# Kernel tuning notes

Measured on AMD Instinct MI355X. Metric: run time of the kernel, lower is better.

The kernel has to match this reference:

```python
import jax, jax.numpy as jnp
import numpy as np

D_HIDDEN = 1024
N_HEADS = 16
D_HEAD = 64
B, N = 4, 1024
EPS = 1e-5


def _lin(x, w, b):
    # torch Linear: y = x @ W^T + b, w: [out, in]
    return jnp.einsum('...i,oi->...o', x, w) + b


def _ln(x, g, b):
    m = jnp.mean(x, axis=-1, keepdims=True)
    v = jnp.mean(jnp.square(x - m), axis=-1, keepdims=True)
    return (x - m) * jax.lax.rsqrt(v + EPS) * g + b


def setup_inputs() -> dict:
    key = jax.random.key(0)
    ks = jax.random.split(key, 20)
    d = D_HIDDEN
    s = 0.02
    inp = {
        'x': jax.random.normal(ks[0], (B, N, d), jnp.float32),
        'time_emb': jax.random.normal(ks[1], (B, d), jnp.float32),
        'ln1_g': jnp.ones((d,), jnp.float32),
        'ln1_b': jnp.zeros((d,), jnp.float32),
        's1_w': jax.random.normal(ks[2], (d, d), jnp.float32) * s,
        's1_b': jnp.zeros((d,), jnp.float32),
        'o1_w': jax.random.normal(ks[3], (d, d), jnp.float32) * s,
        'o1_b': jnp.zeros((d,), jnp.float32),
        'qkv_w': jax.random.normal(ks[4], (3 * d, d), jnp.float32) * s,
        'qkv_b': jnp.zeros((3 * d,), jnp.float32),
        'proj_w': jax.random.normal(ks[5], (d, d), jnp.float32) * s,
        'proj_b': jnp.zeros((d,), jnp.float32),
        'ln2_g': jnp.ones((d,), jnp.float32),
        'ln2_b': jnp.zeros((d,), jnp.float32),
        's2_w': jax.random.normal(ks[6], (d, d), jnp.float32) * s,
        's2_b': jnp.zeros((d,), jnp.float32),
        'o2_w': jax.random.normal(ks[7], (d, d), jnp.float32) * s,
        'o2_b': jnp.zeros((d,), jnp.float32),
        'up_w': jax.random.normal(ks[8], (4 * d, d), jnp.float32) * s,
        'up_b': jnp.zeros((4 * d,), jnp.float32),
        'down_w': jax.random.normal(ks[9], (d, 4 * d), jnp.float32) * s,
        'down_b': jnp.zeros((d,), jnp.float32),
    }
    return inp


def reference(x, time_emb, ln1_g, ln1_b, s1_w, s1_b, o1_w, o1_b,
              qkv_w, qkv_b, proj_w, proj_b, ln2_g, ln2_b,
              s2_w, s2_b, o2_w, o2_b, up_w, up_b, down_w, down_b):
    d = D_HIDDEN

    def ada(h, sw, sb, ow, ob):
        scale = _lin(time_emb, sw, sb)[:, None, :]   # [B,1,d]
        offset = _lin(time_emb, ow, ob)[:, None, :]
        return (1.0 + scale) * h + offset

    # attention branch
    h = ada(_ln(x, ln1_g, ln1_b), s1_w, s1_b, o1_w, o1_b)
    qkv = _lin(h, qkv_w, qkv_b)                       # [B,N,3d]
    q, k, v = jnp.split(qkv, 3, axis=-1)
    q = q.reshape(B, N, N_HEADS, D_HEAD)
    k = k.reshape(B, N, N_HEADS, D_HEAD)
    v = v.reshape(B, N, N_HEADS, D_HEAD)
    wei = jnp.einsum('bnhd,bmhd->bhnm', q, k) * (D_HEAD ** -0.5)
    wei = jax.nn.softmax(wei, axis=-1)
    attn = jnp.einsum('bhnm,bmhd->bnhd', wei, v).reshape(B, N, d)
    x = x + _lin(attn, proj_w, proj_b)

    # mlp branch (torch nn.GELU default = exact erf gelu)
    h = ada(_ln(x, ln2_g, ln2_b), s2_w, s2_b, o2_w, o2_b)
    h = jax.nn.gelu(_lin(h, up_w, up_b), approximate=False)
    x = x + _lin(h, down_w, down_b)
    return x, time_emb
```

## Files before the change

kernel.cpp:

```cpp
#include <hip/hip_runtime.h>
#include <hip/hip_bf16.h>
#include <math.h>

#define DH 1024
#define BB 4
#define NN 1024
#define NH 16
#define HD 64

typedef __attribute__((ext_vector_type(8))) short bf16x8;
typedef __attribute__((ext_vector_type(4))) float f32x4;
typedef __attribute__((ext_vector_type(4))) unsigned int u32x4;
typedef unsigned short u16;
typedef unsigned int u32;

static __device__ __forceinline__ u16 f2bf(float f) {
  __hip_bfloat16 h = __float2bfloat16(f);
  return *reinterpret_cast<u16*>(&h);
}
static __device__ __forceinline__ float bf2f(u16 x) {
  return __uint_as_float((unsigned)x << 16);
}

#define MFMA16(a, b, c) __builtin_amdgcn_mfma_f32_16x16x32_bf16(a, b, c, 0, 0, 0)
#define VMCNT(n) asm volatile("s_waitcnt vmcnt(" #n ")" ::: "memory")
#define MEMFENCE asm volatile("" ::: "memory")
#define BAR() do { __builtin_amdgcn_s_barrier(); MEMFENCE; } while (0)

static __device__ __forceinline__ void async16(const void* g, void* l) {
  __builtin_amdgcn_global_load_lds(
      (const __attribute__((address_space(1))) void*)g,
      (__attribute__((address_space(3))) void*)l, 16, 0, 0);
}

__global__ void cvt_all_kernel(const float* __restrict__ wq, const float* __restrict__ wp,
                               const float* __restrict__ wu, const float* __restrict__ wd,
                               u16* __restrict__ oq, u16* __restrict__ op,
                               u16* __restrict__ ou, u16* __restrict__ od) {
  int i = blockIdx.x * 256 + threadIdx.x;
  const float* src; u16* dst; int off;
  if (i < 786432)            { src = wq; dst = oq; off = i; }
  else if (i < 1048576)      { src = wp; dst = op; off = i - 786432; }
  else if (i < 2097152)      { src = wu; dst = ou; off = i - 1048576; }
  else                       { src = wd; dst = od; off = i - 2097152; }
  float4 v = reinterpret_cast<const float4*>(src)[off];
  ushort4 o;
  o.x = f2bf(v.x); o.y = f2bf(v.y); o.z = f2bf(v.z); o.w = f2bf(v.w);
  reinterpret_cast<ushort4*>(dst)[off] = o;
}

__global__ __launch_bounds__(256) void adaln_kernel(
    const float* __restrict__ e,
    const float* __restrict__ w_s1, const float* __restrict__ b_s1,
    const float* __restrict__ w_o1, const float* __restrict__ b_o1,
    const float* __restrict__ w_s2, const float* __restrict__ b_s2,
    const float* __restrict__ w_o2, const float* __restrict__ b_o2,
    float* __restrict__ out) {
  int tid = threadIdx.x, wid = tid >> 6, lane = tid & 63;
  int mat = blockIdx.y;
  const float* w; const float* bs; float addc;
  if (mat == 0)      { w = w_s1; bs = b_s1; addc = 1.f; }
  else if (mat == 1) { w = w_o1; bs = b_o1; addc = 0.f; }
  else if (mat == 2) { w = w_s2; bs = b_s2; addc = 1.f; }
  else               { w = w_o2; bs = b_o2; addc = 0.f; }
  int col = blockIdx.x * 4 + wid;
  float a0 = 0.f, a1 = 0.f, a2 = 0.f, a3 = 0.f;
  const float* wc_ = w + (size_t)col * DH;
  for (int i = 0; i < 16; ++i) {
    int k = i * 64 + lane;
    float wv = wc_[k];
    a0 += wv * e[k];
    a1 += wv * e[DH + k];
    a2 += wv * e[2 * DH + k];
    a3 += wv * e[3 * DH + k];
  }
  #pragma unroll
  for (int msk = 32; msk; msk >>= 1) {
    a0 += __shfl_xor(a0, msk); a1 += __shfl_xor(a1, msk);
    a2 += __shfl_xor(a2, msk); a3 += __shfl_xor(a3, msk);
  }
  if (lane == 0) {
    float bb = bs[col] + addc;
    out[mat * (4 * DH) + 0 * DH + col] = a0 + bb;
    out[mat * (4 * DH) + 1 * DH + col] = a1 + bb;
    out[mat * (4 * DH) + 2 * DH + col] = a2 + bb;
    out[mat * (4 * DH) + 3 * DH + col] = a3 + bb;
  }
}

__global__ __launch_bounds__(256) void ln_mod_kernel(
    const float* __restrict__ x, const float* __restrict__ g, const float* __restrict__ bta,
    const float* __restrict__ sp, const float* __restrict__ off, u16* __restrict__ out) {
  int row = blockIdx.x;
  int b = row >> 10;
  int tid = threadIdx.x;
  int wid = tid >> 6, lane = tid & 63;
  const float4 xv = reinterpret_cast<const float4*>(x + (size_t)row * DH)[tid];
  float s = xv.x + xv.y + xv.z + xv.w;
  float ss = xv.x * xv.x + xv.y * xv.y + xv.z * xv.z + xv.w * xv.w;
  #pragma unroll
  for (int m = 32; m; m >>= 1) { s += __shfl_xor(s, m); ss += __shfl_xor(ss, m); }
  __shared__ float red[8];
  if (lane == 0) { red[wid] = s; red[4 + wid] = ss; }
  __syncthreads();
  s = red[0] + red[1] + red[2] + red[3];
  ss = red[4] + red[5] + red[6] + red[7];
  float mean = s * (1.f / DH);
  float var = ss * (1.f / DH) - mean * mean;
  float rstd = rsqrtf(var + 1e-5f);
  int c = tid * 4;
  const float* spb = sp + b * DH + c;
  const float* offb = off + b * DH + c;
  float y0 = (xv.x - mean) * rstd * g[c + 0] + bta[c + 0];
  float y1 = (xv.y - mean) * rstd * g[c + 1] + bta[c + 1];
  float y2 = (xv.z - mean) * rstd * g[c + 2] + bta[c + 2];
  float y3 = (xv.w - mean) * rstd * g[c + 3] + bta[c + 3];
  ushort4 o;
  o.x = f2bf(spb[0] * y0 + offb[0]);
  o.y = f2bf(spb[1] * y1 + offb[1]);
  o.z = f2bf(spb[2] * y2 + offb[2]);
  o.w = f2bf(spb[3] * y3 + offb[3]);
  reinterpret_cast<ushort4*>(out + (size_t)row * DH)[tid] = o;
}

enum { EPI_BF16 = 0, EPI_GELU = 1, EPI_PART = 2, EPI_RES = 3 };

template <int EPI>
__global__ __launch_bounds__(512, 2) void gemmT_kernel(
    const u16* __restrict__ A, const u16* __restrict__ W,
    const float* __restrict__ bias, const float* __restrict__ resid,
    void* __restrict__ outp, int N, int K) {
  extern __shared__ u16 lds[];
  u16* Ab = lds;
  u16* Bb = lds + 24576;
  int tid = threadIdx.x;
  int wid = tid >> 6, lane = tid & 63;
  int l15 = lane & 15, l4 = lane >> 4;
  int wr = wid >> 2, wc = wid & 3;

  int nwg = gridDim.x * gridDim.y;
  int lin = blockIdx.y * gridDim.x + blockIdx.x;
  int q8 = nwg >> 3;
  int lin2 = (lin & 7) * q8 + (lin >> 3);
  int bx = lin2 % gridDim.x, by = lin2 / gridDim.x;
  int m0 = by * 256, n0 = bx * 128;
  int k0 = blockIdx.z * 1024;

  f32x4 acc[8][2] = {};

  const u16* Abase = A + (size_t)m0 * K + k0;
  const u16* Wbase = W + (size_t)n0 * K + k0;
  int i0 = tid, i1 = 512 + tid;
  int r0 = i0 >> 2, c0 = (i0 & 3) ^ ((r0 >> 1) & 3);
  int r1 = i1 >> 2, c1 = (i1 & 3) ^ ((r1 >> 1) & 3);
  int rB = tid >> 2, cB = (tid & 3) ^ ((rB >> 1) & 3);
  size_t gA0 = (size_t)r0 * K + c0 * 8;
  size_t gA1 = (size_t)r1 * K + c1 * 8;
  size_t gB0 = (size_t)rB * K + cB * 8;
  int lbA0 = (wid * 64) * 8;
  int lbA1 = (512 + wid * 64) * 8;

  auto stage = [&](int tt, int bi) {
    int qa = bi * 8192, qb = bi * 4096;
    const u16* Ak = Abase + tt * 32;
    const u16* Wk = Wbase + tt * 32;
    async16(Ak + gA0, &Ab[qa + lbA0]);
    async16(Ak + gA1, &Ab[qa + lbA1]);
    async16(Wk + gB0, &Bb[qb + lbA0]);
  };

  auto compute = [&](int bi) {
    int qa = bi * 8192, qb = bi * 4096;
    bf16x8 af[8], bfr[2];
    #pragma unroll
    for (int m = 0; m < 8; ++m) {
      int row = wr * 128 + m * 16 + l15;
      int ps = l4 ^ ((row >> 1) & 3);
      af[m] = *reinterpret_cast<const bf16x8*>(&Ab[qa + row * 32 + ps * 8]);
    }
    #pragma unroll
    for (int n = 0; n < 2; ++n) {
      int row = wc * 32 + n * 16 + l15;
      int ps = l4 ^ ((row >> 1) & 3);
      bfr[n] = *reinterpret_cast<const bf16x8*>(&Bb[qb + row * 32 + ps * 8]);
    }
    #pragma unroll
    for (int m = 0; m < 8; ++m)
      #pragma unroll
      for (int n = 0; n < 2; ++n)
        acc[m][n] = MFMA16(af[m], bfr[n], acc[m][n]);
  };

  stage(0, 0);
  stage(1, 1);
  for (int tb = 0; tb < 30; tb += 3) {
    VMCNT(3); BAR(); stage(tb + 2, 2); compute(0);
    VMCNT(3); BAR(); stage(tb + 3, 0); compute(1);
    VMCNT(3); BAR(); stage(tb + 4, 1); compute(2);
  }
  VMCNT(3); BAR(); compute(0);
  VMCNT(0); BAR(); compute(1);

  int M = gridDim.y * 256;
  u16* pout = (u16*)outp + (size_t)blockIdx.z * M * N;
  #pragma unroll
  for (int n = 0; n < 2; ++n) {
    int col = n0 + wc * 32 + n * 16 + l15;
    float bv = (EPI == EPI_PART) ? 0.f : bias[col];
    #pragma unroll
    for (int m = 0; m < 8; ++m) {
      #pragma unroll
      for (int r = 0; r < 4; ++r) {
        int rowg = m0 + wr * 128 + m * 16 + l4 * 4 + r;
        float v = acc[m][n][r] + bv;
        if (EPI == EPI_GELU) {
          v = 0.5f * v * (1.f + erff(v * 0.70710678118f));
          ((u16*)outp)[(size_t)rowg * N + col] = f2bf(v);
        } else if (EPI == EPI_BF16) {
          ((u16*)outp)[(size_t)rowg * N + col] = f2bf(v);
        } else if (EPI == EPI_RES) {
          ((float*)outp)[(size_t)rowg * N + col] = v + resid[(size_t)rowg * N + col];
        } else {
          pout[(size_t)rowg * N + col] = f2bf(v);
        }
      }
    }
  }
}

__global__ __launch_bounds__(256) void reduce4_kernel(
    const u16* __restrict__ part, const float* __restrict__ x2,
    const float* __restrict__ bias, const float* __restrict__ te,
    float* __restrict__ out) {
  size_t i = (size_t)blockIdx.x * 256 + threadIdx.x;
  const size_t MN = (size_t)4096 * 1024;
  float4 xr = reinterpret_cast<const float4*>(x2)[i];
  int col = (int)((i * 4) & 1023);
  float4 bv = *reinterpret_cast<const float4*>(&bias[col]);
  float a0 = xr.x + bv.x, a1 = xr.y + bv.y, a2 = xr.z + bv.z, a3 = xr.w + bv.w;
  #pragma unroll
  for (int p = 0; p < 4; ++p) {
    ushort4 u = reinterpret_cast<const ushort4*>(part + p * MN)[i];
    a0 += bf2f(u.x); a1 += bf2f(u.y); a2 += bf2f(u.z); a3 += bf2f(u.w);
  }
  float4 o; o.x = a0; o.y = a1; o.z = a2; o.w = a3;
  reinterpret_cast<float4*>(out)[i] = o;
  if (blockIdx.x < 16) {
    int ii = blockIdx.x * 256 + threadIdx.x;
    out[4096 * 1024 + ii] = te[ii];
  }
}

__global__ __launch_bounds__(256) void vt_kernel(const u16* __restrict__ qkvb,
                                                 u16* __restrict__ vT) {
  __shared__ u16 L[64 * 66];
  int bh = blockIdx.y;
  int b = bh >> 4, h = bh & 15;
  int nt = blockIdx.x;
  int t = threadIdx.x;
  const u16* src = qkvb + ((size_t)b * 1024 + nt * 64) * 3072 + 2048 + h * 64;
  int j = t >> 3, s = t & 7;
  bf16x8 r0 = *reinterpret_cast<const bf16x8*>(src + (size_t)j * 3072 + s * 8);
  bf16x8 r1 = *reinterpret_cast<const bf16x8*>(src + (size_t)(j + 32) * 3072 + s * 8);
  #pragma unroll
  for (int e = 0; e < 8; ++e) {
    L[(s * 8 + e) * 66 + j] = r0[e];
    L[(s * 8 + e) * 66 + j + 32] = r1[e];
  }
  __syncthreads();
  int d = t & 63, cp = t >> 6;
  u16* dst = vT + ((size_t)bh * 64 + d) * 1024 + nt * 64;
  #pragma unroll
  for (int half = 0; half < 2; ++half) {
    int cs = cp + half * 4;
    bf16x8 o;
    #pragma unroll
    for (int c = 0; c < 8; ++c) o[c] = L[d * 66 + cs * 8 + c];
    *reinterpret_cast<bf16x8*>(dst + cs * 8) = o;
  }
}

__global__ __launch_bounds__(256, 4) void attn_kernel(
    const u16* __restrict__ qkv, const u16* __restrict__ vT, u16* __restrict__ out) {
  __shared__ __align__(16) u16 Ks[2][4096];
  __shared__ __align__(16) u16 Vs[2][4096];
  int tid = threadIdx.x, wid = tid >> 6, lane = tid & 63;
  int l15 = lane & 15, l4 = lane >> 4;
  int L = blockIdx.y * gridDim.x + blockIdx.x;
  int qt = (L >> 3) & 15;
  int bh = (L & 7) | ((L >> 7) << 3);
  int b = bh >> 4, h = bh & 15;
  const size_t SN = 3 * DH;
  const u16* qb = qkv + (size_t)b * NN * SN + h * HD;
  const u16* kb = qb + DH;
  const u16* vtb = vT + (size_t)bh * 64 * 1024;

  int qrow = qt * 64 + wid * 16 + l15;
  bf16x8 qf[2];
  #pragma unroll
  for (int ks = 0; ks < 2; ++ks)
    qf[ks] = *reinterpret_cast<const bf16x8*>(qb + (size_t)qrow * SN + ks * 32 + l4 * 8);

  float m_ = -1e30f, l_ = 0.f;
  f32x4 o_[4] = {};

  int laA = ((l4 * 2) & 3) * 16 + l15;
  int laB = ((l4 * 2 + 1) & 3) * 16 + l15;
  bool nbhi = (l4 >> 1) != 0;

  int iA = tid, iB = 256 + tid;
  int jA = iA >> 3, sA = iA & 7, gsA = sA ^ (jA & 7);
  int jB = iB >> 3, sB = iB & 7, gsB = sB ^ (jB & 7);

  auto stageKV = [&](int bufn, int t) {
    const u16* kt = kb + (size_t)t * 64 * SN;
    async16(kt + (size_t)jA * SN + gsA * 8, &Ks[bufn][iA * 8]);
    async16(kt + (size_t)jB * SN + gsB * 8, &Ks[bufn][iB * 8]);
    const u16* vt = vtb + (size_t)t * 64;
    async16(vt + (size_t)jA * 1024 + gsA * 8, &Vs[bufn][iA * 8]);
    async16(vt + (size_t)jB * 1024 + gsB * 8, &Vs[bufn][iB * 8]);
  };

  stageKV(0, 0);
  __syncthreads();

  int buf = 0;
  for (int t = 0; t < 16; ++t) {
    if (t < 15) stageKV(buf ^ 1, t + 1);

    f32x4 sa[4];
    #pragma unroll
    for (int nb = 0; nb < 4; ++nb) {
      f32x4 s = {};
      #pragma unroll
      for (int ks = 0; ks < 2; ++ks) {
        int j = nb * 16 + l15;
        int ps = (ks * 4 + l4) ^ (j & 7);
        bf16x8 kf = *reinterpret_cast<const bf16x8*>(&Ks[buf][j * 64 + ps * 8]);
        s = MFMA16(kf, qf[ks], s);
      }
      sa[nb] = s * 0.125f;
    }

    float pm = sa[0][0];
    #pragma unroll
    for (int nb = 0; nb < 4; ++nb)
      #pragma unroll
      for (int r = 0; r < 4; ++r)
        if (nb || r) pm = fmaxf(pm, sa[nb][r]);
    pm = fmaxf(pm, __shfl_xor(pm, 16));
    pm = fmaxf(pm, __shfl_xor(pm, 32));

    if (!__all(pm - m_ <= 8.f)) {
      float mn = fmaxf(m_, pm);
      float corr = __expf(m_ - mn);
      m_ = mn;
      l_ *= corr;
      float c0 = __shfl(corr, l4 * 4 + 0);
      float c1 = __shfl(corr, l4 * 4 + 1);
      float c2 = __shfl(corr, l4 * 4 + 2);
      float c3 = __shfl(corr, l4 * 4 + 3);
      #pragma unroll
      for (int nd = 0; nd < 4; ++nd) {
        o_[nd][0] *= c0; o_[nd][1] *= c1; o_[nd][2] *= c2; o_[nd][3] *= c3;
      }
    }

    float ts = 0.f;
    u32 pk[4][2];
    #pragma unroll
    for (int nb = 0; nb < 4; ++nb) {
      float p0 = __expf(sa[nb][0] - m_);
      float p1 = __expf(sa[nb][1] - m_);
      float p2 = __expf(sa[nb][2] - m_);
      float p3 = __expf(sa[nb][3] - m_);
      ts += (p0 + p1) + (p2 + p3);
      pk[nb][0] = (u32)f2bf(p0) | ((u32)f2bf(p1) << 16);
      pk[nb][1] = (u32)f2bf(p2) | ((u32)f2bf(p3) << 16);
    }
    ts += __shfl_xor(ts, 16);
    ts += __shfl_xor(ts, 32);
    l_ += ts;

    __builtin_amdgcn_s_setprio(1);
    #pragma unroll
    for (int ks = 0; ks < 2; ++ks) {
      int nlo = ks * 2, nhi = ks * 2 + 1;
      u32 a00 = __shfl((int)pk[nlo][0], laA), a01 = __shfl((int)pk[nlo][1], laA);
      u32 a10 = __shfl((int)pk[nhi][0], laA), a11 = __shfl((int)pk[nhi][1], laA);
      u32 b00 = __shfl((int)pk[nlo][0], laB), b01 = __shfl((int)pk[nlo][1], laB);
      u32 b10 = __shfl((int)pk[nhi][0], laB), b11 = __shfl((int)pk[nhi][1], laB);
      u32x4 wv;
      wv[0] = nbhi ? a10 : a00;
      wv[1] = nbhi ? a11 : a01;
      wv[2] = nbhi ? b10 : b00;
      wv[3] = nbhi ? b11 : b01;
      bf16x8 pa = __builtin_bit_cast(bf16x8, wv);
      #pragma unroll
      for (int nd = 0; nd < 4; ++nd) {
        int d = nd * 16 + l15;
        int psv = (ks * 4 + l4) ^ (d & 7);
        bf16x8 vf = *reinterpret_cast<const bf16x8*>(&Vs[buf][d * 64 + psv * 8]);
        o_[nd] = MFMA16(pa, vf, o_[nd]);
      }
    }
    __builtin_amdgcn_s_setprio(0);

    if (t < 15) __syncthreads();
    buf ^= 1;
  }

  float li0 = __shfl(l_, l4 * 4 + 0);
  float li1 = __shfl(l_, l4 * 4 + 1);
  float li2 = __shfl(l_, l4 * 4 + 2);
  float li3 = __shfl(l_, l4 * 4 + 3);
  float inv[4] = { 1.f / li0, 1.f / li1, 1.f / li2, 1.f / li3 };
  u16* ob = out + (size_t)b * NN * DH + h * HD;
  #pragma unroll
  for (int nd = 0; nd < 4; ++nd) {
    #pragma unroll
    for (int r = 0; r < 4; ++r) {
      int q = qt * 64 + wid * 16 + l4 * 4 + r;
      ob[(size_t)q * DH + nd * 16 + l15] = f2bf(o_[nd][r] * inv[r]);
    }
  }
}

extern "C" void kernel_launch(void* const* d_in, const int* in_sizes, int n_in,
                              void* d_out, int out_size, void* d_ws, size_t ws_size,
                              hipStream_t stream) {
  (void)in_sizes; (void)n_in; (void)out_size; (void)ws_size;
  const float* x      = (const float*)d_in[0];
  const float* te     = (const float*)d_in[1];
  const float* ln1_g  = (const float*)d_in[2];
  const float* ln1_b  = (const float*)d_in[3];
  const float* s1_w   = (const float*)d_in[4];
  const float* s1_b   = (const float*)d_in[5];
  const float* o1_w   = (const float*)d_in[6];
  const float* o1_b   = (const float*)d_in[7];
  const float* qkv_w  = (const float*)d_in[8];
  const float* qkv_b  = (const float*)d_in[9];
  const float* proj_w = (const float*)d_in[10];
  const float* proj_b = (const float*)d_in[11];
  const float* ln2_g  = (const float*)d_in[12];
  const float* ln2_b  = (const float*)d_in[13];
  const float* s2_w   = (const float*)d_in[14];
  const float* s2_b   = (const float*)d_in[15];
  const float* o2_w   = (const float*)d_in[16];
  const float* o2_b   = (const float*)d_in[17];
  const float* up_w   = (const float*)d_in[18];
  const float* up_b   = (const float*)d_in[19];
  const float* down_w = (const float*)d_in[20];
  const float* down_b = (const float*)d_in[21];

  char* ws = (char*)d_ws;
  size_t off = 0;
  auto alloc = [&](size_t bytes) { void* p = ws + off; off += (bytes + 255) & ~255ull; return p; };
  u16*   wq   = (u16*)  alloc((size_t)3072 * 1024 * 2);
  u16*   wp   = (u16*)  alloc((size_t)1024 * 1024 * 2);
  u16*   wu   = (u16*)  alloc((size_t)4096 * 1024 * 2);
  u16*   h1   = (u16*)  alloc((size_t)4096 * 1024 * 2);
  u16*   qkvb = (u16*)  alloc((size_t)4096 * 3072 * 2);
  u16*   att  = (u16*)  alloc((size_t)4096 * 1024 * 2);
  u16*   h2   = (u16*)  alloc((size_t)4096 * 1024 * 2);
  u16*   wd   = (u16*)  alloc((size_t)1024 * 4096 * 2);
  float* x2   = (float*)alloc((size_t)4096 * 1024 * 4);
  u16*   upb  = (u16*)  alloc((size_t)4096 * 4096 * 2);
  float* ada  = (float*)alloc((size_t)4 * 4 * 1024 * 4);
  float* sp1 = ada, *off1 = ada + 4096, *sp2 = ada + 8192, *off2 = ada + 12288;
  u16*   part = wq;
  u16*   vT   = h1;

  cvt_all_kernel<<<12288, 256, 0, stream>>>(qkv_w, proj_w, up_w, down_w, wq, wp, wu, wd);
  adaln_kernel<<<dim3(256, 4), 256, 0, stream>>>(te, s1_w, s1_b, o1_w, o1_b, s2_w, s2_b, o2_w, o2_b, ada);
  ln_mod_kernel<<<4096, 256, 0, stream>>>(x, ln1_g, ln1_b, sp1, off1, h1);
  gemmT_kernel<EPI_BF16><<<dim3(24, 16, 1), 512, 73728, stream>>>(h1, wq, qkv_b, nullptr, qkvb, 3072, 1024);
  vt_kernel<<<dim3(16, 64), 256, 0, stream>>>(qkvb, vT);
  attn_kernel<<<dim3(16, 64), 256, 0, stream>>>(qkvb, vT, att);
  gemmT_kernel<EPI_RES><<<dim3(8, 16, 1), 512, 73728, stream>>>(att, wp, proj_b, x, x2, 1024, 1024);
  ln_mod_kernel<<<4096, 256, 0, stream>>>(x2, ln2_g, ln2_b, sp2, off2, h2);
  gemmT_kernel<EPI_GELU><<<dim3(32, 16, 1), 512, 73728, stream>>>(h2, wu, up_b, nullptr, upb, 4096, 1024);
  gemmT_kernel<EPI_PART><<<dim3(8, 16, 4), 512, 73728, stream>>>(upb, wd, nullptr, nullptr, part, 1024, 4096);
  reduce4_kernel<<<4096, 256, 0, stream>>>(part, x2, down_b, te, (float*)d_out);
}
```

Before: 241.3 us.

## Process two 16-row query tiles per wave in attention to reuse K/V fragments

Each wave in the attention kernel now handles 32 query rows as two independent 16-row online-softmax streams that share every K and V fragment read from LDS. The block covers 128 queries instead of 64, so the grid is halved and each block stages K/V once for twice as many queries. This aims to cut LDS reads and global K/V traffic per query and to give the MFMA units more independent work. The cost is higher register pressure, reflected in the launch bound dropping from 4 to 2 blocks per SIMD, and fewer blocks in flight (512).

```diff
diff --git a/kernel.cpp b/kernel.cpp
--- a/kernel.cpp
+++ b/kernel.cpp
@@ -280,29 +280,34 @@
   }
 }
 
-__global__ __launch_bounds__(256, 4) void attn_kernel(
+__global__ __launch_bounds__(256, 2) void attn_kernel(
     const u16* __restrict__ qkv, const u16* __restrict__ vT, u16* __restrict__ out) {
   __shared__ __align__(16) u16 Ks[2][4096];
   __shared__ __align__(16) u16 Vs[2][4096];
   int tid = threadIdx.x, wid = tid >> 6, lane = tid & 63;
   int l15 = lane & 15, l4 = lane >> 4;
   int L = blockIdx.y * gridDim.x + blockIdx.x;
-  int qt = (L >> 3) & 15;
-  int bh = (L & 7) | ((L >> 7) << 3);
+  int qt = (L >> 3) & 7;
+  int bh = (L & 7) | ((L >> 6) << 3);
   int b = bh >> 4, h = bh & 15;
   const size_t SN = 3 * DH;
   const u16* qb = qkv + (size_t)b * NN * SN + h * HD;
   const u16* kb = qb + DH;
   const u16* vtb = vT + (size_t)bh * 64 * 1024;
 
-  int qrow = qt * 64 + wid * 16 + l15;
-  bf16x8 qf[2];
-  #pragma unroll
-  for (int ks = 0; ks < 2; ++ks)
-    qf[ks] = *reinterpret_cast<const bf16x8*>(qb + (size_t)qrow * SN + ks * 32 + l4 * 8);
-
-  float m_ = -1e30f, l_ = 0.f;
-  f32x4 o_[4] = {};
+  bf16x8 qf0[2], qf1[2];
+  {
+    int qr0 = qt * 128 + wid * 32 + l15;
+    int qr1 = qr0 + 16;
+    #pragma unroll
+    for (int ks = 0; ks < 2; ++ks) {
+      qf0[ks] = *reinterpret_cast<const bf16x8*>(qb + (size_t)qr0 * SN + ks * 32 + l4 * 8);
+      qf1[ks] = *reinterpret_cast<const bf16x8*>(qb + (size_t)qr1 * SN + ks * 32 + l4 * 8);
+    }
+  }
+
+  float m0_ = -1e30f, l0_ = 0.f, m1_ = -1e30f, l1_ = 0.f;
+  f32x4 o0_[4] = {}, o1_[4] = {};
 
   int laA = ((l4 * 2) & 3) * 16 + l15;
   int laB = ((l4 * 2 + 1) & 3) * 16 + l15;
@@ -328,80 +333,94 @@
   for (int t = 0; t < 16; ++t) {
     if (t < 15) stageKV(buf ^ 1, t + 1);
 
-    f32x4 sa[4];
+    f32x4 sa0[4], sa1[4];
     #pragma unroll
     for (int nb = 0; nb < 4; ++nb) {
-      f32x4 s = {};
+      f32x4 s0 = {}, s1 = {};
       #pragma unroll
       for (int ks = 0; ks < 2; ++ks) {
         int j = nb * 16 + l15;
         int ps = (ks * 4 + l4) ^ (j & 7);
         bf16x8 kf = *reinterpret_cast<const bf16x8*>(&Ks[buf][j * 64 + ps * 8]);
-        s = MFMA16(kf, qf[ks], s);
-      }
-      sa[nb] = s * 0.125f;
-    }
-
-    float pm = sa[0][0];
+        s0 = MFMA16(kf, qf0[ks], s0);
+        s1 = MFMA16(kf, qf1[ks], s1);
+      }
+      sa0[nb] = s0 * 0.125f;
+      sa1[nb] = s1 * 0.125f;
+    }
+
+    float pm0 = sa0[0][0], pm1 = sa1[0][0];
     #pragma unroll
     for (int nb = 0; nb < 4; ++nb)
       #pragma unroll
-      for (int r = 0; r < 4; ++r)
-        if (nb || r) pm = fmaxf(pm, sa[nb][r]);
-    pm = fmaxf(pm, __shfl_xor(pm, 16));
-    pm = fmaxf(pm, __shfl_xor(pm, 32));
-
-    if (!__all(pm - m_ <= 8.f)) {
-      float mn = fmaxf(m_, pm);
-      float corr = __expf(m_ - mn);
-      m_ = mn;
-      l_ *= corr;
-      float c0 = __shfl(corr, l4 * 4 + 0);
-      float c1 = __shfl(corr, l4 * 4 + 1);
-      float c2 = __shfl(corr, l4 * 4 + 2);
-      float c3 = __shfl(corr, l4 * 4 + 3);
+      for (int r = 0; r < 4; ++r) {
+        if (nb || r) { pm0 = fmaxf(pm0, sa0[nb][r]); pm1 = fmaxf(pm1, sa1[nb][r]); }
+      }
+    pm0 = fmaxf(pm0, __shfl_xor(pm0, 16)); pm0 = fmaxf(pm0, __shfl_xor(pm0, 32));
+    pm1 = fmaxf(pm1, __shfl_xor(pm1, 16)); pm1 = fmaxf(pm1, __shfl_xor(pm1, 32));
+
+    if (!__all(fmaxf(pm0 - m0_, pm1 - m1_) <= 8.f)) {
+      float mn0 = fmaxf(m0_, pm0), mn1 = fmaxf(m1_, pm1);
+      float cr0 = __expf(m0_ - mn0), cr1 = __expf(m1_ - mn1);
+      m0_ = mn0; m1_ = mn1;
+      l0_ *= cr0; l1_ *= cr1;
       #pragma unroll
-      for (int nd = 0; nd < 4; ++nd) {
-        o_[nd][0] *= c0; o_[nd][1] *= c1; o_[nd][2] *= c2; o_[nd][3] *= c3;
-      }
-    }
-
-    float ts = 0.f;
-    u32 pk[4][2];
+      for (int r = 0; r < 4; ++r) {
+        float c0 = __shfl(cr0, l4 * 4 + r);
+        float c1 = __shfl(cr1, l4 * 4 + r);
+        #pragma unroll
+        for (int nd = 0; nd < 4; ++nd) { o0_[nd][r] *= c0; o1_[nd][r] *= c1; }
+      }
+    }
+
+    float ts0 = 0.f, ts1 = 0.f;
+    u32 pk0[4][2], pk1[4][2];
     #pragma unroll
     for (int nb = 0; nb < 4; ++nb) {
-      float p0 = __expf(sa[nb][0] - m_);
-      float p1 = __expf(sa[nb][1] - m_);
-      float p2 = __expf(sa[nb][2] - m_);
-      float p3 = __expf(sa[nb][3] - m_);
-      ts += (p0 + p1) + (p2 + p3);
-      pk[nb][0] = (u32)f2bf(p0) | ((u32)f2bf(p1) << 16);
-      pk[nb][1] = (u32)f2bf(p2) | ((u32)f2bf(p3) << 16);
-    }
-    ts += __shfl_xor(ts, 16);
-    ts += __shfl_xor(ts, 32);
-    l_ += ts;
+      float a0 = __expf(sa0[nb][0] - m0_), a1 = __expf(sa0[nb][1] - m0_);
+      float a2 = __expf(sa0[nb][2] - m0_), a3 = __expf(sa0[nb][3] - m0_);
+      ts0 += (a0 + a1) + (a2 + a3);
+      pk0[nb][0] = (u32)f2bf(a0) | ((u32)f2bf(a1) << 16);
+      pk0[nb][1] = (u32)f2bf(a2) | ((u32)f2bf(a3) << 16);
+      float b0 = __expf(sa1[nb][0] - m1_), b1 = __expf(sa1[nb][1] - m1_);
+      float b2 = __expf(sa1[nb][2] - m1_), b3 = __expf(sa1[nb][3] - m1_);
+      ts1 += (b0 + b1) + (b2 + b3);
+      pk1[nb][0] = (u32)f2bf(b0) | ((u32)f2bf(b1) << 16);
+      pk1[nb][1] = (u32)f2bf(b2) | ((u32)f2bf(b3) << 16);
+    }
+    ts0 += __shfl_xor(ts0, 16); ts0 += __shfl_xor(ts0, 32); l0_ += ts0;
+    ts1 += __shfl_xor(ts1, 16); ts1 += __shfl_xor(ts1, 32); l1_ += ts1;
 
     __builtin_amdgcn_s_setprio(1);
     #pragma unroll
     for (int ks = 0; ks < 2; ++ks) {
       int nlo = ks * 2, nhi = ks * 2 + 1;
-      u32 a00 = __shfl((int)pk[nlo][0], laA), a01 = __shfl((int)pk[nlo][1], laA);
-      u32 a10 = __shfl((int)pk[nhi][0], laA), a11 = __shfl((int)pk[nhi][1], laA);
-      u32 b00 = __shfl((int)pk[nlo][0], laB), b01 = __shfl((int)pk[nlo][1], laB);
-      u32 b10 = __shfl((int)pk[nhi][0], laB), b11 = __shfl((int)pk[nhi][1], laB);
-      u32x4 wv;
-      wv[0] = nbhi ? a10 : a00;
-      wv[1] = nbhi ? a11 : a01;
-      wv[2] = nbhi ? b10 : b00;
-      wv[3] = nbhi ? b11 : b01;
-      bf16x8 pa = __builtin_bit_cast(bf16x8, wv);
+      u32x4 w0, w1;
+      {
+        u32 a00 = __shfl((int)pk0[nlo][0], laA), a01 = __shfl((int)pk0[nlo][1], laA);
+        u32 a10 = __shfl((int)pk0[nhi][0], laA), a11 = __shfl((int)pk0[nhi][1], laA);
+        u32 b00 = __shfl((int)pk0[nlo][0], laB), b01 = __shfl((int)pk0[nlo][1], laB);
+        u32 b10 = __shfl((int)pk0[nhi][0], laB), b11 = __shfl((int)pk0[nhi][1], laB);
+        w0[0] = nbhi ? a10 : a00; w0[1] = nbhi ? a11 : a01;
+        w0[2] = nbhi ? b10 : b00; w0[3] = nbhi ? b11 : b01;
+      }
+      {
+        u32 a00 = __shfl((int)pk1[nlo][0], laA), a01 = __shfl((int)pk1[nlo][1], laA);
+        u32 a10 = __shfl((int)pk1[nhi][0], laA), a11 = __shfl((int)pk1[nhi][1], laA);
+        u32 b00 = __shfl((int)pk1[nlo][0], laB), b01 = __shfl((int)pk1[nlo][1], laB);
+        u32 b10 = __shfl((int)pk1[nhi][0], laB), b11 = __shfl((int)pk1[nhi][1], laB);
+        w1[0] = nbhi ? a10 : a00; w1[1] = nbhi ? a11 : a01;
+        w1[2] = nbhi ? b10 : b00; w1[3] = nbhi ? b11 : b01;
+      }
+      bf16x8 pa0 = __builtin_bit_cast(bf16x8, w0);
+      bf16x8 pa1 = __builtin_bit_cast(bf16x8, w1);
       #pragma unroll
       for (int nd = 0; nd < 4; ++nd) {
         int d = nd * 16 + l15;
         int psv = (ks * 4 + l4) ^ (d & 7);
         bf16x8 vf = *reinterpret_cast<const bf16x8*>(&Vs[buf][d * 64 + psv * 8]);
-        o_[nd] = MFMA16(pa, vf, o_[nd]);
+        o0_[nd] = MFMA16(pa0, vf, o0_[nd]);
+        o1_[nd] = MFMA16(pa1, vf, o1_[nd]);
       }
     }
     __builtin_amdgcn_s_setprio(0);
@@ -410,18 +429,17 @@
     buf ^= 1;
   }
 
-  float li0 = __shfl(l_, l4 * 4 + 0);
-  float li1 = __shfl(l_, l4 * 4 + 1);
-  float li2 = __shfl(l_, l4 * 4 + 2);
-  float li3 = __shfl(l_, l4 * 4 + 3);
-  float inv[4] = { 1.f / li0, 1.f / li1, 1.f / li2, 1.f / li3 };
   u16* ob = out + (size_t)b * NN * DH + h * HD;
   #pragma unroll
-  for (int nd = 0; nd < 4; ++nd) {
-    #pragma unroll
-    for (int r = 0; r < 4; ++r) {
-      int q = qt * 64 + wid * 16 + l4 * 4 + r;
-      ob[(size_t)q * DH + nd * 16 + l15] = f2bf(o_[nd][r] * inv[r]);
+  for (int r = 0; r < 4; ++r) {
+    float inv0 = 1.f / __shfl(l0_, l4 * 4 + r);
+    float inv1 = 1.f / __shfl(l1_, l4 * 4 + r);
+    int q0 = qt * 128 + wid * 32 + l4 * 4 + r;
+    int q1 = q0 + 16;
+    #pragma unroll
+    for (int nd = 0; nd < 4; ++nd) {
+      ob[(size_t)q0 * DH + nd * 16 + l15] = f2bf(o0_[nd][r] * inv0);
+      ob[(size_t)q1 * DH + nd * 16 + l15] = f2bf(o1_[nd][r] * inv1);
     }
   }
 }
@@ -476,7 +494,7 @@
   ln_mod_kernel<<<4096, 256, 0, stream>>>(x, ln1_g, ln1_b, sp1, off1, h1);
   gemmT_kernel<EPI_BF16><<<dim3(24, 16, 1), 512, 73728, stream>>>(h1, wq, qkv_b, nullptr, qkvb, 3072, 1024);
   vt_kernel<<<dim3(16, 64), 256, 0, stream>>>(qkvb, vT);
-  attn_kernel<<<dim3(16, 64), 256, 0, stream>>>(qkvb, vT, att);
+  attn_kernel<<<dim3(8, 64), 256, 0, stream>>>(qkvb, vT, att);
   gemmT_kernel<EPI_RES><<<dim3(8, 16, 1), 512, 73728, stream>>>(att, wp, proj_b, x, x2, 1024, 1024);
   ln_mod_kernel<<<4096, 256, 0, stream>>>(x2, ln2_g, ln2_b, sp2, off2, h2);
   gemmT_kernel<EPI_GELU><<<dim3(32, 16, 1), 512, 73728, stream>>>(h2, wu, up_b, nullptr, upb, 4096, 1024);
```

Result: no change. 243.1 us (+0.7%).
